# Kernel tuning notes

Hardware: AMD Instinct MI355X
Metric: run time of the kernel (lower is better)

The kernel has to match this reference:

```python
import jax, jax.numpy as jnp
import numpy as np

ALPHA = 1.5
A = 0.5
BANDWIDTH = 1.0
SPHERE_RADIUS = 1.0
HIDDEN = 1024
HEAD = 64
EPS_ACOS = 1e-07
EPS_NORM = 1e-12  # torch F.normalize clamp_min eps


def _l2norm(v):
    # F.normalize(v, p=2, dim=-1)
    n = jnp.sqrt(jnp.sum(v * v, axis=-1, keepdims=True))
    return v / jnp.maximum(n, EPS_NORM)


def setup_inputs() -> dict:
    key = jax.random.key(0)
    ks = jax.random.split(key, 7)
    B, S = 8, 2048
    s = 1.0 / np.sqrt(HIDDEN)
    return {
        "x": jax.random.normal(ks[0], (B, S, HIDDEN), dtype=jnp.float32),
        "Wq": jax.random.uniform(ks[1], (HIDDEN, HEAD), jnp.float32, -s, s),
        "bq": jax.random.uniform(ks[2], (HEAD,), jnp.float32, -s, s),
        "Wk": jax.random.uniform(ks[3], (HIDDEN, HEAD), jnp.float32, -s, s),
        "bk": jax.random.uniform(ks[4], (HEAD,), jnp.float32, -s, s),
        "Wv": jax.random.uniform(ks[5], (HIDDEN, HEAD), jnp.float32, -s, s),
        "bv": jax.random.uniform(ks[6], (HEAD,), jnp.float32, -s, s),
    }


def reference(x, Wq, bq, Wk, bk, Wv, bv):
    # q,k,v: [B,S,HEAD], L2-normalized along feature axis
    q = _l2norm(jnp.einsum("bsh,hd->bsd", x, Wq) + bq)
    k = _l2norm(jnp.einsum("bsh,hd->bsd", x, Wk) + bk)
    v = _l2norm(jnp.einsum("bsh,hd->bsd", x, Wv) + bv)

    # geodesic distance on sphere: [B,S,S]
    cos = jnp.einsum("bqd,bkd->bqk", q, k)
    g_dist = jnp.arccos(jnp.clip(cos, -1.0 + EPS_ACOS, 1.0 - EPS_ACOS)) * SPHERE_RADIUS

    # alpha < 2 -> power-law score
    score = (1.0 + g_dist / jnp.sqrt(BANDWIDTH)) ** (-HEAD - ALPHA)

    # dual degree normalization (a != 0): diag(row^-a) @ S @ diag(col^-a),
    # expressed as broadcast row/col scaling (same math, no diag_embed matmuls)
    r = jnp.sum(score, axis=-1) ** (-A)  # [B,Sq]
    c = jnp.sum(score, axis=-2) ** (-A)  # [B,Sk]
    k_tilde = r[..., :, None] * score * c[..., None, :]

    # L1 normalize over key axis (F.normalize p=1): entries are positive
    denom = jnp.maximum(jnp.sum(jnp.abs(k_tilde), axis=-1, keepdims=True), EPS_NORM)
    probs = k_tilde / denom

    out = jnp.einsum("bqk,bkd->bqd", probs, v)
    return (out, probs)
```

## Files before the change

kernel.cpp:

```cpp
#include <hip/hip_runtime.h>
#include <math.h>

#define BB 8
#define SS 2048
#define HH 1024
#define DD 64
#define NCV 65

typedef __attribute__((ext_vector_type(8))) short bf16x8;
typedef __attribute__((ext_vector_type(4))) float f32x4;
typedef __attribute__((ext_vector_type(16))) float f32x16;

#define MFMA16(a, b, c) __builtin_amdgcn_mfma_f32_16x16x32_bf16(a, b, c, 0, 0, 0)
#define MFMA32(a, b, c) __builtin_amdgcn_mfma_f32_32x32x16_bf16(a, b, c, 0, 0, 0)

__device__ __forceinline__ ushort bf16rne(float f) {
    uint u = __float_as_uint(f);
    uint r = (u + 0x7FFFu + ((u >> 16) & 1u)) >> 16;
    return (ushort)r;
}
__device__ __forceinline__ float bf2f(ushort h) {
    return __uint_as_float(((uint)h) << 16);
}

__device__ __forceinline__ float score_fn(float cosv) {
    float ax = fminf(fabsf(cosv), 1.0f - 1e-7f);
    float p = fmaf(ax, -0.0012624911f, 0.0066700901f);
    p = fmaf(ax, p, -0.0170881256f);
    p = fmaf(ax, p, 0.0308918810f);
    p = fmaf(ax, p, -0.0501743046f);
    p = fmaf(ax, p, 0.0889789874f);
    p = fmaf(ax, p, -0.2145988016f);
    p = fmaf(ax, p, 1.5707963050f);
    float r = sqrtf(1.0f - ax) * p;
    float g = (cosv >= 0.0f) ? r : (3.14159265358979f - r);
    return exp2f(-65.5f * log2f(1.0f + g));
}

__global__ __launch_bounds__(256) void k_prep(
    const float* __restrict__ Wq, const float* __restrict__ Wk, const float* __restrict__ Wv,
    const float* __restrict__ bq, const float* __restrict__ bk, const float* __restrict__ bv,
    ushort* __restrict__ Whi, ushort* __restrict__ Wlo, float* __restrict__ bcat)
{
    const int n = blockIdx.x;
    const int m = n >> 6, d = n & 63;
    const float* W = (m == 0) ? Wq : (m == 1 ? Wk : Wv);
    #pragma unroll
    for (int i = 0; i < 4; ++i) {
        int j = i * 256 + threadIdx.x;
        float f = W[(size_t)j * DD + d];
        ushort h = bf16rne(f);
        Whi[(size_t)n * HH + j] = h;
        Wlo[(size_t)n * HH + j] = bf16rne(f - bf2f(h));
    }
    if (n == 0 && threadIdx.x < 192) {
        int t = threadIdx.x, mm = t >> 6, dd = t & 63;
        const float* b = (mm == 0) ? bq : (mm == 1 ? bk : bv);
        bcat[t] = b[dd];
    }
}

__global__ __launch_bounds__(256) void k_projmm(
    const float* __restrict__ x, const ushort* __restrict__ Whi,
    const ushort* __restrict__ Wlo, const float* __restrict__ bcat,
    ushort* __restrict__ qh, ushort* __restrict__ ql,
    ushort* __restrict__ kh, ushort* __restrict__ kl,
    float* __restrict__ vw)
{
    __shared__ __align__(16) char smem[32 * 193 * 4];
    __shared__ float rns[96];
    __shared__ float bsh[192];
    ushort* xhi = (ushort*)smem;
    ushort* xlo = xhi + 32 * 128;
    float* ctile = (float*)smem;

    const int t = threadIdx.x;
    const int lane = t & 63;
    const int wid = t >> 6;
    const int row0 = blockIdx.x * 32;
    if (t < 192) bsh[t] = bcat[t];

    f32x4 acc[2][3];
    #pragma unroll
    for (int ar = 0; ar < 2; ++ar)
        #pragma unroll
        for (int bc = 0; bc < 3; ++bc)
            acc[ar][bc] = (f32x4){0.f, 0.f, 0.f, 0.f};

    for (int ch = 0; ch < 8; ++ch) {
        const int j0 = ch * 128;
        __syncthreads();
        #pragma unroll
        for (int i = 0; i < 2; ++i) {
            int u = i * 256 + t;
            int row = u >> 4, uc = u & 15;
            const float* xp = &x[(size_t)(row0 + row) * HH + j0 + uc * 8];
            float4 a = *(const float4*)xp;
            float4 b = *(const float4*)(xp + 4);
            float fs[8] = {a.x, a.y, a.z, a.w, b.x, b.y, b.z, b.w};
            bf16x8 hv, lv;
            #pragma unroll
            for (int e = 0; e < 8; ++e) {
                ushort h = bf16rne(fs[e]);
                hv[e] = (short)h;
                lv[e] = (short)bf16rne(fs[e] - bf2f(h));
            }
            int su = uc ^ (row & 7);
            *(bf16x8*)(xhi + row * 128 + su * 8) = hv;
            *(bf16x8*)(xlo + row * 128 + su * 8) = lv;
        }
        __syncthreads();
        #pragma unroll
        for (int ks = 0; ks < 4; ++ks) {
            bf16x8 ah[2], al[2], bh[3], bl[3];
            #pragma unroll
            for (int ar = 0; ar < 2; ++ar) {
                int row = ar * 16 + (lane & 15);
                int su = (ks * 4 + (lane >> 4)) ^ (row & 7);
                ah[ar] = *(const bf16x8*)(xhi + row * 128 + su * 8);
                al[ar] = *(const bf16x8*)(xlo + row * 128 + su * 8);
            }
            const int koff = j0 + ks * 32 + (lane >> 4) * 8;
            #pragma unroll
            for (int bc = 0; bc < 3; ++bc) {
                int n = wid * 48 + bc * 16 + (lane & 15);
                bh[bc] = *(const bf16x8*)(Whi + (size_t)n * HH + koff);
                bl[bc] = *(const bf16x8*)(Wlo + (size_t)n * HH + koff);
            }
            #pragma unroll
            for (int ar = 0; ar < 2; ++ar)
                #pragma unroll
                for (int bc = 0; bc < 3; ++bc) {
                    acc[ar][bc] = MFMA16(ah[ar], bh[bc], acc[ar][bc]);
                    acc[ar][bc] = MFMA16(ah[ar], bl[bc], acc[ar][bc]);
                    acc[ar][bc] = MFMA16(al[ar], bh[bc], acc[ar][bc]);
                }
        }
    }
    __syncthreads();
    #pragma unroll
    for (int ar = 0; ar < 2; ++ar)
        #pragma unroll
        for (int bc = 0; bc < 3; ++bc) {
            int n = wid * 48 + bc * 16 + (lane & 15);
            #pragma unroll
            for (int r = 0; r < 4; ++r) {
                int row = ar * 16 + (lane >> 4) * 4 + r;
                ctile[row * 193 + n] = acc[ar][bc][r];
            }
        }
    __syncthreads();
    if (t < 96) {
        int mat = t >> 5, row = t & 31;
        float ss = 0.f;
        #pragma unroll 8
        for (int d = 0; d < 64; ++d) {
            float v = ctile[row * 193 + mat * 64 + d] + bsh[mat * 64 + d];
            ss = fmaf(v, v, ss);
        }
        rns[t] = 1.0f / fmaxf(sqrtf(ss), 1e-12f);
    }
    __syncthreads();
    #pragma unroll
    for (int i = 0; i < 24; ++i) {
        int idx = i * 256 + t;
        int row = idx / 192;
        int n = idx - row * 192;
        float v = (ctile[row * 193 + n] + bsh[n]) * rns[(n >> 6) * 32 + row];
        size_t off = (size_t)(row0 + row) * DD + (n & 63);
        if (n < 64) {
            ushort h = bf16rne(v);
            qh[off] = h; ql[off] = bf16rne(v - bf2f(h));
        } else if (n < 128) {
            ushort h = bf16rne(v);
            kh[off] = h; kl[off] = bf16rne(v - bf2f(h));
        } else {
            vw[off] = v;
        }
    }
}

#define K_LOAD(H0,H1,H2,H3,L0,L1,L2,L3, KT) { \
    const ushort* kp = kh + (size_t)(b * SS + kbase + (KT) * 32 + qrow) * DD + kg; \
    const ushort* lp = kl + (size_t)(b * SS + kbase + (KT) * 32 + qrow) * DD + kg; \
    H0 = *(const bf16x8*)(kp);      L0 = *(const bf16x8*)(lp); \
    H1 = *(const bf16x8*)(kp + 16); L1 = *(const bf16x8*)(lp + 16); \
    H2 = *(const bf16x8*)(kp + 32); L2 = *(const bf16x8*)(lp + 32); \
    H3 = *(const bf16x8*)(kp + 48); L3 = *(const bf16x8*)(lp + 48); }

#define K_COMPUTE(H0,H1,H2,H3,L0,L1,L2,L3, KT) { \
    f32x16 acc = Z16; \
    acc = MFMA32(H0, qbh0, acc); acc = MFMA32(H0, qbl0, acc); acc = MFMA32(L0, qbh0, acc); \
    acc = MFMA32(H1, qbh1, acc); acc = MFMA32(H1, qbl1, acc); acc = MFMA32(L1, qbh1, acc); \
    acc = MFMA32(H2, qbh2, acc); acc = MFMA32(H2, qbl2, acc); acc = MFMA32(L2, qbh2, acc); \
    acc = MFMA32(H3, qbh3, acc); acc = MFMA32(H3, qbl3, acc); acc = MFMA32(L3, qbh3, acc); \
    const int kloc = kbase + (KT) * 32 + hi4; \
    uint2 wv; \
    wv.x = (uint)bf16rne(score_fn(acc[0]))  | ((uint)bf16rne(score_fn(acc[1]))  << 16); \
    wv.y = (uint)bf16rne(score_fn(acc[2]))  | ((uint)bf16rne(score_fn(acc[3]))  << 16); \
    *(uint2*)(srow + kloc) = wv; \
    wv.x = (uint)bf16rne(score_fn(acc[4]))  | ((uint)bf16rne(score_fn(acc[5]))  << 16); \
    wv.y = (uint)bf16rne(score_fn(acc[6]))  | ((uint)bf16rne(score_fn(acc[7]))  << 16); \
    *(uint2*)(srow + kloc + 8) = wv; \
    wv.x = (uint)bf16rne(score_fn(acc[8]))  | ((uint)bf16rne(score_fn(acc[9]))  << 16); \
    wv.y = (uint)bf16rne(score_fn(acc[10])) | ((uint)bf16rne(score_fn(acc[11])) << 16); \
    *(uint2*)(srow + kloc + 16) = wv; \
    wv.x = (uint)bf16rne(score_fn(acc[12])) | ((uint)bf16rne(score_fn(acc[13])) << 16); \
    wv.y = (uint)bf16rne(score_fn(acc[14])) | ((uint)bf16rne(score_fn(acc[15])) << 16); \
    *(uint2*)(srow + kloc + 24) = wv; }

__global__ __launch_bounds__(256, 4) void k_score(
    const ushort* __restrict__ qh, const ushort* __restrict__ ql,
    const ushort* __restrict__ kh, const ushort* __restrict__ kl,
    ushort* __restrict__ scrS)
{
    const int t = threadIdx.x;
    const int lane = t & 63;
    const int w = t >> 6;
    const int bid = blockIdx.x;
    const int b  = bid >> 8;
    const int q0 = ((bid >> 2) & 63) * 32;
    const int kbase = (bid & 3) * 512 + w * 128;
    const int qrow = lane & 31;
    const int kg = (lane >> 5) * 8;
    const int hi4 = (lane >> 5) * 4;
    const f32x16 Z16 = {0.f,0.f,0.f,0.f,0.f,0.f,0.f,0.f,0.f,0.f,0.f,0.f,0.f,0.f,0.f,0.f};

    const size_t qoff = (size_t)(b * SS + q0 + qrow) * DD + kg;
    bf16x8 qbh0 = *(const bf16x8*)(qh + qoff);
    bf16x8 qbh1 = *(const bf16x8*)(qh + qoff + 16);
    bf16x8 qbh2 = *(const bf16x8*)(qh + qoff + 32);
    bf16x8 qbh3 = *(const bf16x8*)(qh + qoff + 48);
    bf16x8 qbl0 = *(const bf16x8*)(ql + qoff);
    bf16x8 qbl1 = *(const bf16x8*)(ql + qoff + 16);
    bf16x8 qbl2 = *(const bf16x8*)(ql + qoff + 32);
    bf16x8 qbl3 = *(const bf16x8*)(ql + qoff + 48);
    ushort* srow = scrS + (size_t)(b * SS + q0 + qrow) * 4096 + 2048;

    bf16x8 xh0, xh1, xh2, xh3, xl0, xl1, xl2, xl3;
    bf16x8 yh0, yh1, yh2, yh3, yl0, yl1, yl2, yl3;
    K_LOAD(xh0,xh1,xh2,xh3,xl0,xl1,xl2,xl3, 0)
    K_LOAD(yh0,yh1,yh2,yh3,yl0,yl1,yl2,yl3, 1)
    K_COMPUTE(xh0,xh1,xh2,xh3,xl0,xl1,xl2,xl3, 0)
    K_LOAD(xh0,xh1,xh2,xh3,xl0,xl1,xl2,xl3, 2)
    K_COMPUTE(yh0,yh1,yh2,yh3,yl0,yl1,yl2,yl3, 1)
    K_LOAD(yh0,yh1,yh2,yh3,yl0,yl1,yl2,yl3, 3)
    K_COMPUTE(xh0,xh1,xh2,xh3,xl0,xl1,xl2,xl3, 2)
    K_COMPUTE(yh0,yh1,yh2,yh3,yl0,yl1,yl2,yl3, 3)
}

__global__ __launch_bounds__(256) void k_csum_cvc(
    const ushort* __restrict__ scrS, const float* __restrict__ vw,
    ushort* __restrict__ cvT)
{
    __shared__ float cls[32][64];
    __shared__ float csh[64];
    __shared__ float vsT[64][65];
    const int t = threadIdx.x;
    const int b = blockIdx.x >> 5;
    const int k0 = (blockIdx.x & 31) * 64;

    {
        const int tq = t >> 3, tk = t & 7;
        float colacc[8];
        #pragma unroll
        for (int e = 0; e < 8; ++e) colacc[e] = 0.f;
        #pragma unroll 4
        for (int it = 0; it < 64; ++it) {
            int q = it * 32 + tq;
            bf16x8 s8 = *(const bf16x8*)(scrS + (size_t)(b * SS + q) * 4096 + 2048 + k0 + tk * 8);
            #pragma unroll
            for (int e = 0; e < 8; ++e) colacc[e] += bf2f((ushort)s8[e]);
        }
        #pragma unroll
        for (int e = 0; e < 8; ++e) cls[tq][tk * 8 + e] = colacc[e];
    }
    __syncthreads();
    if (t < 64) {
        float s = 0.f;
        #pragma unroll
        for (int tq = 0; tq < 32; ++tq) s += cls[tq][t];
        csh[t] = 1.0f / sqrtf(s);
    }
    {
        const int j = t & 63, rr = t >> 6;
        #pragma unroll
        for (int it = 0; it < 16; ++it) {
            int kk = it * 4 + rr;
            vsT[j][kk] = vw[(size_t)(b * SS + k0 + kk) * DD + j];
        }
    }
    __syncthreads();
    {
        const int kk4 = (t & 15) * 4;
        #pragma unroll
        for (int jt = 0; jt < 4; ++jt) {
            int j = jt * 16 + (t >> 4);
            uint2 wv;
            wv.x = (uint)bf16rne(csh[kk4 + 0] * vsT[j][kk4 + 0])
                 | ((uint)bf16rne(csh[kk4 + 1] * vsT[j][kk4 + 1]) << 16);
            wv.y = (uint)bf16rne(csh[kk4 + 2] * vsT[j][kk4 + 2])
                 | ((uint)bf16rne(csh[kk4 + 3] * vsT[j][kk4 + 3]) << 16);
            *(uint2*)(cvT + ((size_t)b * NCV + j) * SS + k0 + kk4) = wv;
        }
        if (t < 16) {
            uint2 wv;
            wv.x = (uint)bf16rne(csh[t * 4 + 0]) | ((uint)bf16rne(csh[t * 4 + 1]) << 16);
            wv.y = (uint)bf16rne(csh[t * 4 + 2]) | ((uint)bf16rne(csh[t * 4 + 3]) << 16);
            *(uint2*)(cvT + ((size_t)b * NCV + 64) * SS + k0 + t * 4) = wv;
        }
    }
}

__global__ __launch_bounds__(256, 4) void k_final(
    const ushort* __restrict__ scrS, const ushort* __restrict__ cvT,
    float* __restrict__ probs, float* __restrict__ out)
{
    __shared__ float nred[32][64];
    __shared__ float dPart[4][32];
    __shared__ float dInv[32];
    const int t = threadIdx.x;
    const int lane = t & 63;
    const int w = t >> 6;
    const int b = blockIdx.x >> 6;
    const int q0 = (blockIdx.x & 63) * 32;
    const int kbase = w * 512;
    const int qrow = lane & 31;
    const int kg = (lane >> 5) * 8;
    const f32x16 Z16 = {0.f,0.f,0.f,0.f,0.f,0.f,0.f,0.f,0.f,0.f,0.f,0.f,0.f,0.f,0.f,0.f};

    #pragma unroll
    for (int i = 0; i < 8; ++i) ((float*)nred)[t + i * 256] = 0.f;
    __syncthreads();

    const ushort* cslice = cvT + (size_t)b * NCV * SS;
    const ushort* cbrow = cslice + (size_t)64 * SS;
    const ushort* srow = scrS + (size_t)(b * SS + q0 + qrow) * 4096 + 2048;

    float dacc = 0.f;
    f32x16 n0 = Z16, n1 = Z16;

    #pragma unroll 4
    for (int ch = 0; ch < 32; ++ch) {
        const int kc = kbase + ch * 16 + kg;
        bf16x8 s8 = *(const bf16x8*)(srow + kc);
        bf16x8 c8 = *(const bf16x8*)(cbrow + kc);
        bf16x8 b0 = *(const bf16x8*)(cslice + (size_t)qrow * SS + kc);
        bf16x8 b1 = *(const bf16x8*)(cslice + (size_t)(32 + qrow) * SS + kc);
        #pragma unroll
        for (int e = 0; e < 8; ++e)
            dacc = fmaf(bf2f((ushort)s8[e]), bf2f((ushort)c8[e]), dacc);
        n0 = MFMA32(s8, b0, n0);
        n1 = MFMA32(s8, b1, n1);
    }
    {
        float d = dacc;
        d += __shfl_xor(d, 32, 64);
        if (lane < 32) dPart[w][lane] = d;
    }
    __syncthreads();
    if (t < 32) dInv[t] = 1.0f / (dPart[0][t] + dPart[1][t] + dPart[2][t] + dPart[3][t]);
    #pragma unroll
    for (int r = 0; r < 16; ++r) {
        int q = (r & 3) + 8 * (r >> 2) + 4 * (lane >> 5);
        atomicAdd(&nred[q][qrow], n0[r]);
        atomicAdd(&nred[q][32 + qrow], n1[r]);
    }
    __syncthreads();
    {
        int q = t >> 3, d0 = (t & 7) * 8;
        float di = dInv[q];
        float4 o0, o1;
        o0.x = nred[q][d0 + 0] * di; o0.y = nred[q][d0 + 1] * di;
        o0.z = nred[q][d0 + 2] * di; o0.w = nred[q][d0 + 3] * di;
        o1.x = nred[q][d0 + 4] * di; o1.y = nred[q][d0 + 5] * di;
        o1.z = nred[q][d0 + 6] * di; o1.w = nred[q][d0 + 7] * di;
        float* op = &out[(size_t)(b * SS + q0 + q) * DD + d0];
        *(float4*)op = o0;
        *(float4*)(op + 4) = o1;
    }
    float cf[8];
    {
        bf16x8 c8 = *(const bf16x8*)(cbrow + t * 8);
        #pragma unroll
        for (int e = 0; e < 8; ++e) cf[e] = bf2f((ushort)c8[e]);
    }
#define P_STORE(S8, DI, RR) { \
    float4 o0, o1; \
    o0.x = bf2f((ushort)S8[0]) * cf[0] * DI; \
    o0.y = bf2f((ushort)S8[1]) * cf[1] * DI; \
    o0.z = bf2f((ushort)S8[2]) * cf[2] * DI; \
    o0.w = bf2f((ushort)S8[3]) * cf[3] * DI; \
    o1.x = bf2f((ushort)S8[4]) * cf[4] * DI; \
    o1.y = bf2f((ushort)S8[5]) * cf[5] * DI; \
    o1.z = bf2f((ushort)S8[6]) * cf[6] * DI; \
    o1.w = bf2f((ushort)S8[7]) * cf[7] * DI; \
    float* prow = probs + (size_t)(b * SS + q0 + (RR)) * SS + t * 8; \
    *(float4*)prow = o0; \
    *(float4*)(prow + 4) = o1; }

    #pragma unroll
    for (int r0 = 0; r0 < 32; r0 += 4) {
        bf16x8 sA = *(const bf16x8*)(scrS + (size_t)(b * SS + q0 + r0 + 0) * 4096 + 2048 + t * 8);
        bf16x8 sB = *(const bf16x8*)(scrS + (size_t)(b * SS + q0 + r0 + 1) * 4096 + 2048 + t * 8);
        bf16x8 sC = *(const bf16x8*)(scrS + (size_t)(b * SS + q0 + r0 + 2) * 4096 + 2048 + t * 8);
        bf16x8 sD = *(const bf16x8*)(scrS + (size_t)(b * SS + q0 + r0 + 3) * 4096 + 2048 + t * 8);
        float dA = dInv[r0 + 0], dB = dInv[r0 + 1], dC = dInv[r0 + 2], dD = dInv[r0 + 3];
        __syncthreads();
        P_STORE(sA, dA, r0 + 0)
        P_STORE(sB, dB, r0 + 1)
        P_STORE(sC, dC, r0 + 2)
        P_STORE(sD, dD, r0 + 3)
    }
}

extern "C" void kernel_launch(void* const* d_in, const int* in_sizes, int n_in,
                              void* d_out, int out_size, void* d_ws, size_t ws_size,
                              hipStream_t stream)
{
    const float* x  = (const float*)d_in[0];
    const float* Wq = (const float*)d_in[1];
    const float* bq = (const float*)d_in[2];
    const float* Wk = (const float*)d_in[3];
    const float* bk = (const float*)d_in[4];
    const float* Wv = (const float*)d_in[5];
    const float* bv = (const float*)d_in[6];

    float* out   = (float*)d_out;
    float* probs = out + (size_t)BB * SS * DD;
    ushort* scrS = (ushort*)probs;

    const size_t NQ = (size_t)BB * SS * DD;
    ushort* qh    = (ushort*)d_ws;
    ushort* ql    = qh + NQ;
    ushort* kh    = ql + NQ;
    ushort* kl    = kh + NQ;
    float*  vw    = (float*)(kl + NQ);
    ushort* cvT   = (ushort*)(vw + NQ);
    ushort* Whi   = cvT + (size_t)BB * NCV * SS;
    ushort* Wlo   = Whi + (size_t)192 * HH;
    float*  bcat  = (float*)(Wlo + (size_t)192 * HH);

    k_prep    <<<192, 256, 0, stream>>>(Wq, Wk, Wv, bq, bk, bv, Whi, Wlo, bcat);
    k_projmm  <<<512, 256, 0, stream>>>(x, Whi, Wlo, bcat, qh, ql, kh, kl, vw);
    k_score   <<<2048, 256, 0, stream>>>(qh, ql, kh, kl, scrS);
    k_csum_cvc<<<256, 256, 0, stream>>>(scrS, vw, cvT);
    k_final   <<<512, 256, 0, stream>>>(scrS, cvT, probs, out);
}
```

Before: 221.6 us.

## Split column-sum and final kernels into finer-grained, more parallel stages

Result: slower. 227.4 us (+2.6%).

```diff
diff --git a/kernel.cpp b/kernel.cpp
--- a/kernel.cpp
+++ b/kernel.cpp
@@ -249,168 +249,172 @@
     K_COMPUTE(yh0,yh1,yh2,yh3,yl0,yl1,yl2,yl3, 3)
 }
 
-__global__ __launch_bounds__(256) void k_csum_cvc(
-    const ushort* __restrict__ scrS, const float* __restrict__ vw,
-    ushort* __restrict__ cvT)
+__global__ __launch_bounds__(256) void k_csum(
+    const ushort* __restrict__ scrS, float* __restrict__ colsum)
 {
     __shared__ float cls[32][64];
-    __shared__ float csh[64];
-    __shared__ float vsT[64][65];
-    const int t = threadIdx.x;
-    const int b = blockIdx.x >> 5;
-    const int k0 = (blockIdx.x & 31) * 64;
-
-    {
-        const int tq = t >> 3, tk = t & 7;
-        float colacc[8];
-        #pragma unroll
-        for (int e = 0; e < 8; ++e) colacc[e] = 0.f;
-        #pragma unroll 4
-        for (int it = 0; it < 64; ++it) {
-            int q = it * 32 + tq;
-            bf16x8 s8 = *(const bf16x8*)(scrS + (size_t)(b * SS + q) * 4096 + 2048 + k0 + tk * 8);
-            #pragma unroll
-            for (int e = 0; e < 8; ++e) colacc[e] += bf2f((ushort)s8[e]);
-        }
-        #pragma unroll
-        for (int e = 0; e < 8; ++e) cls[tq][tk * 8 + e] = colacc[e];
-    }
+    const int t = threadIdx.x;
+    const int bid = blockIdx.x;
+    const int b  = bid >> 8;
+    const int k0 = ((bid >> 3) & 31) * 64;
+    const int qs = (bid & 7) * 256;
+    const int tq = t >> 3, tk = t & 7;
+    float colacc[8];
+    #pragma unroll
+    for (int e = 0; e < 8; ++e) colacc[e] = 0.f;
+    #pragma unroll 2
+    for (int it = 0; it < 8; ++it) {
+        int q = qs + it * 32 + tq;
+        bf16x8 s8 = *(const bf16x8*)(scrS + (size_t)(b * SS + q) * 4096 + 2048 + k0 + tk * 8);
+        #pragma unroll
+        for (int e = 0; e < 8; ++e) colacc[e] += bf2f((ushort)s8[e]);
+    }
+    #pragma unroll
+    for (int e = 0; e < 8; ++e) cls[tq][tk * 8 + e] = colacc[e];
     __syncthreads();
     if (t < 64) {
         float s = 0.f;
         #pragma unroll
-        for (int tq = 0; tq < 32; ++tq) s += cls[tq][t];
-        csh[t] = 1.0f / sqrtf(s);
-    }
-    {
-        const int j = t & 63, rr = t >> 6;
-        #pragma unroll
-        for (int it = 0; it < 16; ++it) {
-            int kk = it * 4 + rr;
-            vsT[j][kk] = vw[(size_t)(b * SS + k0 + kk) * DD + j];
-        }
-    }
-    __syncthreads();
-    {
-        const int kk4 = (t & 15) * 4;
-        #pragma unroll
-        for (int jt = 0; jt < 4; ++jt) {
-            int j = jt * 16 + (t >> 4);
-            uint2 wv;
-            wv.x = (uint)bf16rne(csh[kk4 + 0] * vsT[j][kk4 + 0])
-                 | ((uint)bf16rne(csh[kk4 + 1] * vsT[j][kk4 + 1]) << 16);
-            wv.y = (uint)bf16rne(csh[kk4 + 2] * vsT[j][kk4 + 2])
-                 | ((uint)bf16rne(csh[kk4 + 3] * vsT[j][kk4 + 3]) << 16);
-            *(uint2*)(cvT + ((size_t)b * NCV + j) * SS + k0 + kk4) = wv;
-        }
-        if (t < 16) {
-            uint2 wv;
-            wv.x = (uint)bf16rne(csh[t * 4 + 0]) | ((uint)bf16rne(csh[t * 4 + 1]) << 16);
-            wv.y = (uint)bf16rne(csh[t * 4 + 2]) | ((uint)bf16rne(csh[t * 4 + 3]) << 16);
-            *(uint2*)(cvT + ((size_t)b * NCV + 64) * SS + k0 + t * 4) = wv;
-        }
-    }
-}
-
-__global__ __launch_bounds__(256, 4) void k_final(
+        for (int i = 0; i < 32; ++i) s += cls[i][t];
+        atomicAdd(&colsum[b * SS + k0 + t], s);
+    }
+}
+
+__global__ __launch_bounds__(256) void k_cvc(
+    const float* __restrict__ vw, const float* __restrict__ colsum,
+    ushort* __restrict__ cvT)
+{
+    __shared__ float vs[128][68];
+    const int t = threadIdx.x;
+    const int b = blockIdx.x >> 4;
+    const int k0 = (blockIdx.x & 15) * 128;
+    #pragma unroll
+    for (int i = 0; i < 8; ++i) {
+        int idx = i * 256 + t;
+        int r = idx >> 4, c4 = idx & 15;
+        float4 v4 = *(const float4*)&vw[(size_t)(b * SS + k0 + r) * DD + c4 * 4];
+        *(float4*)&vs[r][c4 * 4] = v4;
+    }
+    __syncthreads();
+    const int tk = t & 127;
+    const int tj = t >> 7;
+    float c = 1.0f / sqrtf(colsum[b * SS + k0 + tk]);
+    #pragma unroll
+    for (int jj = 0; jj < 32; ++jj) {
+        int j = jj * 2 + tj;
+        cvT[((size_t)b * NCV + j) * SS + k0 + tk] = bf16rne(c * vs[tk][j]);
+    }
+    if (tj == 0) cvT[((size_t)b * NCV + 64) * SS + k0 + tk] = bf16rne(c);
+}
+
+__global__ __launch_bounds__(256, 4) void k_nd(
     const ushort* __restrict__ scrS, const ushort* __restrict__ cvT,
-    float* __restrict__ probs, float* __restrict__ out)
-{
-    __shared__ float nred[32][64];
-    __shared__ float dPart[4][32];
-    __shared__ float dInv[32];
+    float* __restrict__ dinv_g, float* __restrict__ out)
+{
+    __shared__ float nred[16][64];
+    __shared__ float dPart[4][16];
+    __shared__ float dInv[16];
     const int t = threadIdx.x;
     const int lane = t & 63;
     const int w = t >> 6;
-    const int b = blockIdx.x >> 6;
-    const int q0 = (blockIdx.x & 63) * 32;
+    const int b = blockIdx.x >> 7;
+    const int q0 = (blockIdx.x & 127) * 16;
     const int kbase = w * 512;
-    const int qrow = lane & 31;
-    const int kg = (lane >> 5) * 8;
-    const f32x16 Z16 = {0.f,0.f,0.f,0.f,0.f,0.f,0.f,0.f,0.f,0.f,0.f,0.f,0.f,0.f,0.f,0.f};
-
-    #pragma unroll
-    for (int i = 0; i < 8; ++i) ((float*)nred)[t + i * 256] = 0.f;
+    const int qn = lane & 15;
+    const int g = lane >> 4;
+
+    ((float*)nred)[t] = 0.f; ((float*)nred)[t + 256] = 0.f;
+    ((float*)nred)[t + 512] = 0.f; ((float*)nred)[t + 768] = 0.f;
     __syncthreads();
 
     const ushort* cslice = cvT + (size_t)b * NCV * SS;
     const ushort* cbrow = cslice + (size_t)64 * SS;
-    const ushort* srow = scrS + (size_t)(b * SS + q0 + qrow) * 4096 + 2048;
+    const ushort* srow = scrS + (size_t)(b * SS + q0 + qn) * 4096 + 2048;
 
     float dacc = 0.f;
-    f32x16 n0 = Z16, n1 = Z16;
+    f32x4 nacc[4];
+    #pragma unroll
+    for (int ct = 0; ct < 4; ++ct) nacc[ct] = (f32x4){0.f, 0.f, 0.f, 0.f};
 
     #pragma unroll 4
-    for (int ch = 0; ch < 32; ++ch) {
-        const int kc = kbase + ch * 16 + kg;
-        bf16x8 s8 = *(const bf16x8*)(srow + kc);
-        bf16x8 c8 = *(const bf16x8*)(cbrow + kc);
-        bf16x8 b0 = *(const bf16x8*)(cslice + (size_t)qrow * SS + kc);
-        bf16x8 b1 = *(const bf16x8*)(cslice + (size_t)(32 + qrow) * SS + kc);
+    for (int ch = 0; ch < 16; ++ch) {
+        const int ks0 = kbase + ch * 32;
+        bf16x8 s8 = *(const bf16x8*)(srow + ks0 + g * 8);
+        bf16x8 c8 = *(const bf16x8*)(cbrow + ks0 + g * 8);
         #pragma unroll
         for (int e = 0; e < 8; ++e)
             dacc = fmaf(bf2f((ushort)s8[e]), bf2f((ushort)c8[e]), dacc);
-        n0 = MFMA32(s8, b0, n0);
-        n1 = MFMA32(s8, b1, n1);
+        #pragma unroll
+        for (int ct = 0; ct < 4; ++ct) {
+            bf16x8 bfv = *(const bf16x8*)(cslice + (size_t)(ct * 16 + qn) * SS + ks0 + g * 8);
+            nacc[ct] = MFMA16(s8, bfv, nacc[ct]);
+        }
     }
     {
         float d = dacc;
+        d += __shfl_xor(d, 16, 64);
         d += __shfl_xor(d, 32, 64);
-        if (lane < 32) dPart[w][lane] = d;
-    }
-    __syncthreads();
-    if (t < 32) dInv[t] = 1.0f / (dPart[0][t] + dPart[1][t] + dPart[2][t] + dPart[3][t]);
-    #pragma unroll
-    for (int r = 0; r < 16; ++r) {
-        int q = (r & 3) + 8 * (r >> 2) + 4 * (lane >> 5);
-        atomicAdd(&nred[q][qrow], n0[r]);
-        atomicAdd(&nred[q][32 + qrow], n1[r]);
-    }
+        if (lane < 16) dPart[w][lane] = d;
+    }
+    __syncthreads();
+    if (t < 16) {
+        float di = 1.0f / (dPart[0][t] + dPart[1][t] + dPart[2][t] + dPart[3][t]);
+        dInv[t] = di;
+        dinv_g[b * SS + q0 + t] = di;
+    }
+    #pragma unroll
+    for (int ct = 0; ct < 4; ++ct)
+        #pragma unroll
+        for (int r = 0; r < 4; ++r)
+            atomicAdd(&nred[g * 4 + r][ct * 16 + qn], nacc[ct][r]);
     __syncthreads();
     {
-        int q = t >> 3, d0 = (t & 7) * 8;
+        int q = t >> 4, c4 = (t & 15) * 4;
         float di = dInv[q];
-        float4 o0, o1;
-        o0.x = nred[q][d0 + 0] * di; o0.y = nred[q][d0 + 1] * di;
-        o0.z = nred[q][d0 + 2] * di; o0.w = nred[q][d0 + 3] * di;
-        o1.x = nred[q][d0 + 4] * di; o1.y = nred[q][d0 + 5] * di;
-        o1.z = nred[q][d0 + 6] * di; o1.w = nred[q][d0 + 7] * di;
-        float* op = &out[(size_t)(b * SS + q0 + q) * DD + d0];
-        *(float4*)op = o0;
-        *(float4*)(op + 4) = o1;
-    }
+        float4 o;
+        o.x = nred[q][c4] * di;     o.y = nred[q][c4 + 1] * di;
+        o.z = nred[q][c4 + 2] * di; o.w = nred[q][c4 + 3] * di;
+        *(float4*)&out[(size_t)(b * SS + q0 + q) * DD + c4] = o;
+    }
+}
+
+__global__ __launch_bounds__(256) void k_probs(
+    const ushort* __restrict__ scrS, const ushort* __restrict__ cvT,
+    const float* __restrict__ dinv_g, float* __restrict__ probs)
+{
+    const int t = threadIdx.x;
+    const int b = blockIdx.x >> 8;
+    const int r0 = (blockIdx.x & 255) * 8;
+    const ushort* cbrow = cvT + ((size_t)b * NCV + 64) * SS;
+
     float cf[8];
     {
         bf16x8 c8 = *(const bf16x8*)(cbrow + t * 8);
         #pragma unroll
         for (int e = 0; e < 8; ++e) cf[e] = bf2f((ushort)c8[e]);
     }
-#define P_STORE(S8, DI, RR) { \
-    float4 o0, o1; \
-    o0.x = bf2f((ushort)S8[0]) * cf[0] * DI; \
-    o0.y = bf2f((ushort)S8[1]) * cf[1] * DI; \
-    o0.z = bf2f((ushort)S8[2]) * cf[2] * DI; \
-    o0.w = bf2f((ushort)S8[3]) * cf[3] * DI; \
-    o1.x = bf2f((ushort)S8[4]) * cf[4] * DI; \
-    o1.y = bf2f((ushort)S8[5]) * cf[5] * DI; \
-    o1.z = bf2f((ushort)S8[6]) * cf[6] * DI; \
-    o1.w = bf2f((ushort)S8[7]) * cf[7] * DI; \
-    float* prow = probs + (size_t)(b * SS + q0 + (RR)) * SS + t * 8; \
-    *(float4*)prow = o0; \
-    *(float4*)(prow + 4) = o1; }
-
-    #pragma unroll
-    for (int r0 = 0; r0 < 32; r0 += 4) {
-        bf16x8 sA = *(const bf16x8*)(scrS + (size_t)(b * SS + q0 + r0 + 0) * 4096 + 2048 + t * 8);
-        bf16x8 sB = *(const bf16x8*)(scrS + (size_t)(b * SS + q0 + r0 + 1) * 4096 + 2048 + t * 8);
-        bf16x8 sC = *(const bf16x8*)(scrS + (size_t)(b * SS + q0 + r0 + 2) * 4096 + 2048 + t * 8);
-        bf16x8 sD = *(const bf16x8*)(scrS + (size_t)(b * SS + q0 + r0 + 3) * 4096 + 2048 + t * 8);
-        float dA = dInv[r0 + 0], dB = dInv[r0 + 1], dC = dInv[r0 + 2], dD = dInv[r0 + 3];
-        __syncthreads();
-        P_STORE(sA, dA, r0 + 0)
-        P_STORE(sB, dB, r0 + 1)
-        P_STORE(sC, dC, r0 + 2)
-        P_STORE(sD, dD, r0 + 3)
+    bf16x8 s8[8];
+    float di[8];
+    #pragma unroll
+    for (int r = 0; r < 8; ++r) {
+        s8[r] = *(const bf16x8*)(scrS + (size_t)(b * SS + r0 + r) * 4096 + 2048 + t * 8);
+        di[r] = dinv_g[b * SS + r0 + r];
+    }
+    __syncthreads();
+    #pragma unroll
+    for (int r = 0; r < 8; ++r) {
+        float4 o0, o1;
+        o0.x = bf2f((ushort)s8[r][0]) * cf[0] * di[r];
+        o0.y = bf2f((ushort)s8[r][1]) * cf[1] * di[r];
+        o0.z = bf2f((ushort)s8[r][2]) * cf[2] * di[r];
+        o0.w = bf2f((ushort)s8[r][3]) * cf[3] * di[r];
+        o1.x = bf2f((ushort)s8[r][4]) * cf[4] * di[r];
+        o1.y = bf2f((ushort)s8[r][5]) * cf[5] * di[r];
+        o1.z = bf2f((ushort)s8[r][6]) * cf[6] * di[r];
+        o1.w = bf2f((ushort)s8[r][7]) * cf[7] * di[r];
+        float* prow = probs + (size_t)(b * SS + r0 + r) * SS + t * 8;
+        *(float4*)prow = o0;
+        *(float4*)(prow + 4) = o1;
     }
 }
 
@@ -436,14 +440,19 @@
     ushort* kh    = ql + NQ;
     ushort* kl    = kh + NQ;
     float*  vw    = (float*)(kl + NQ);
-    ushort* cvT   = (ushort*)(vw + NQ);
+    float*  colsum = vw + NQ;
+    float*  dinv  = colsum + BB * SS;
+    ushort* cvT   = (ushort*)(dinv + BB * SS);
     ushort* Whi   = cvT + (size_t)BB * NCV * SS;
     ushort* Wlo   = Whi + (size_t)192 * HH;
     float*  bcat  = (float*)(Wlo + (size_t)192 * HH);
 
-    k_prep    <<<192, 256, 0, stream>>>(Wq, Wk, Wv, bq, bk, bv, Whi, Wlo, bcat);
-    k_projmm  <<<512, 256, 0, stream>>>(x, Whi, Wlo, bcat, qh, ql, kh, kl, vw);
-    k_score   <<<2048, 256, 0, stream>>>(qh, ql, kh, kl, scrS);
-    k_csum_cvc<<<256, 256, 0, stream>>>(scrS, vw, cvT);
-    k_final   <<<512, 256, 0, stream>>>(scrS, cvT, probs, out);
-}
+    hipMemsetAsync(colsum, 0, BB * SS * sizeof(float), stream);
+    k_prep  <<<192, 256, 0, stream>>>(Wq, Wk, Wv, bq, bk, bv, Whi, Wlo, bcat);
+    k_projmm<<<512, 256, 0, stream>>>(x, Whi, Wlo, bcat, qh, ql, kh, kl, vw);
+    k_score <<<2048, 256, 0, stream>>>(qh, ql, kh, kl, scrS);
+    k_csum  <<<2048, 256, 0, stream>>>(scrS, colsum);
+    k_cvc   <<<128, 256, 0, stream>>>(vw, colsum, cvT);
+    k_nd    <<<1024, 256, 0, stream>>>(scrS, cvT, dinv, out);
+    k_probs <<<2048, 256, 0, stream>>>(scrS, cvT, dinv, probs);
+}
```
